# Performance work log

Hardware: AMD Instinct MI355X
Metric: run time of the kernel (lower is better)

Reference implementation:

```python
import jax, jax.numpy as jnp
import numpy as np

M = 262144      # total tokens
K = 64          # n_channels (input dim)
N = 64          # expert_size (output dim)
E = 8           # n_experts


def setup_inputs() -> dict:
    key = jax.random.key(0)
    k1, k2, k3 = jax.random.split(key, 3)
    x = jax.random.normal(k1, (M, K), dtype=jnp.float32)
    sel = jax.random.randint(k2, (M,), 0, E, dtype=jnp.int32)
    w = jax.random.normal(k3, (E, K, N), dtype=jnp.float32)
    return {"x": x, "sel": sel, "w": w}


def reference(x, sel, w):
    # cvmm: out[m] = x[m] @ w[sel[m]]  (per-token expert GEMM)
    # Loop over the small fixed expert set; accumulate masked dense GEMMs
    # instead of materializing w[sel] ([M,K,N], which would be huge).
    E_ = w.shape[0]
    out = jnp.zeros((x.shape[0], w.shape[2]), dtype=x.dtype)
    for e in range(E_):
        mask = (sel == e)[:, None]           # [M,1]
        out = out + jnp.where(mask, x @ w[e], jnp.zeros((), x.dtype))
    return out
```

## Files before the change

### kernel.cpp

```cpp
#include <hip/hip_runtime.h>


typedef __bf16 bf16x8 __attribute__((ext_vector_type(8)));
typedef float floatx4 __attribute__((ext_vector_type(4)));

#define MT_PER_BLOCK 16

__global__ __launch_bounds__(256, 4) void cvmm_kernel(
    const float* __restrict__ x,
    const int* __restrict__ sel,
    const float* __restrict__ w,
    float* __restrict__ out,
    int M)
{
    const int lane = threadIdx.x & 63;
    const int wave = threadIdx.x >> 6;
    const int n0   = wave << 4;
    const int quad = lane >> 4;
    const int l16  = lane & 15;

    bf16x8 bfrag[8][2];
#pragma unroll
    for (int e = 0; e < 8; ++e) {
#pragma unroll
        for (int t = 0; t < 2; ++t) {
            const float* wp = w + ((e * 64 + t * 32 + quad * 8) * 64) + (n0 + l16);
#pragma unroll
            for (int j = 0; j < 8; ++j) {
                bfrag[e][t][j] = (__bf16)wp[j * 64];
            }
        }
    }

    bf16x8 zf;
#pragma unroll
    for (int j = 0; j < 8; ++j) zf[j] = (__bf16)0.0f;

    const int mt0 = blockIdx.x * MT_PER_BLOCK;

    for (int i = 0; i < MT_PER_BLOCK; ++i) {
        const int m0 = (mt0 + i) << 4;
        if (m0 >= M) break;

        const int s = sel[m0 + l16];

        const float* xp = x + (size_t)(m0 + l16) * 64 + quad * 8;
        floatx4 a0lo = *(const floatx4*)(xp);
        floatx4 a0hi = *(const floatx4*)(xp + 4);
        floatx4 a1lo = *(const floatx4*)(xp + 32);
        floatx4 a1hi = *(const floatx4*)(xp + 36);

        bf16x8 af0, af1;
#pragma unroll
        for (int j = 0; j < 4; ++j) {
            af0[j]     = (__bf16)a0lo[j];
            af0[j + 4] = (__bf16)a0hi[j];
            af1[j]     = (__bf16)a1lo[j];
            af1[j + 4] = (__bf16)a1hi[j];
        }

        floatx4 c = {0.0f, 0.0f, 0.0f, 0.0f};

#pragma unroll
        for (int e = 0; e < 8; ++e) {
            const bool ok = (s == e);
            bf16x8 a0m = ok ? af0 : zf;
            bf16x8 a1m = ok ? af1 : zf;
            c = __builtin_amdgcn_mfma_f32_16x16x32_bf16(a0m, bfrag[e][0], c, 0, 0, 0);
            c = __builtin_amdgcn_mfma_f32_16x16x32_bf16(a1m, bfrag[e][1], c, 0, 0, 0);
        }

        float* op = out + (size_t)(m0 + quad * 4) * 64 + n0 + l16;
#pragma unroll
        for (int r = 0; r < 4; ++r) {
            op[(size_t)r * 64] = c[r];
        }
    }
}

extern "C" void kernel_launch(void* const* d_in, const int* in_sizes, int n_in,
                              void* d_out, int out_size, void* d_ws, size_t ws_size,
                              hipStream_t stream) {
    const float* x   = (const float*)d_in[0];
    const int*   sel = (const int*)d_in[1];
    const float* w   = (const float*)d_in[2];
    float*       out = (float*)d_out;

    const int M = in_sizes[0] / 64;
    const int mtiles = M / 16;
    const int blocks = (mtiles + MT_PER_BLOCK - 1) / MT_PER_BLOCK;

    cvmm_kernel<<<blocks, 256, 0, stream>>>(x, sel, w, out, M);
}
```

Baseline: 149.5 us.

## Prefetch next tile, split MFMA accumulators, use nontemporal stores, shrink per-block tiles

The loop now issues the loads for the next 16-row tile of x and sel before the current tile's MFMAs, so memory latency overlaps with compute. The MFMA chain is split into two independent accumulators to break the serial dependency, and outputs are written with nontemporal stores. Tiles per block drop from 16 to 4 and launch bounds move from 4 to 3, which means more blocks, each reloading the expert weights into registers. The bounds check on M was removed, so correctness relies on M being a multiple of 64.

```diff
diff --git a/kernel.cpp b/kernel.cpp
--- a/kernel.cpp
+++ b/kernel.cpp
@@ -4,9 +4,9 @@
 typedef __bf16 bf16x8 __attribute__((ext_vector_type(8)));
 typedef float floatx4 __attribute__((ext_vector_type(4)));
 
-#define MT_PER_BLOCK 16
+#define MT 4
 
-__global__ __launch_bounds__(256, 4) void cvmm_kernel(
+__global__ __launch_bounds__(256, 3) void cvmm_kernel(
     const float* __restrict__ x,
     const int* __restrict__ sel,
     const float* __restrict__ w,
@@ -36,44 +36,60 @@
 #pragma unroll
     for (int j = 0; j < 8; ++j) zf[j] = (__bf16)0.0f;
 
-    const int mt0 = blockIdx.x * MT_PER_BLOCK;
+    const int mt0 = blockIdx.x * MT;
 
-    for (int i = 0; i < MT_PER_BLOCK; ++i) {
-        const int m0 = (mt0 + i) << 4;
-        if (m0 >= M) break;
+    floatx4 pa0, pa1, pa2, pa3;
+    int ps;
+    {
+        const int m0 = mt0 << 4;
+        const float* xp = x + (size_t)(m0 + l16) * 64 + quad * 8;
+        pa0 = *(const floatx4*)(xp);
+        pa1 = *(const floatx4*)(xp + 4);
+        pa2 = *(const floatx4*)(xp + 32);
+        pa3 = *(const floatx4*)(xp + 36);
+        ps  = sel[m0 + l16];
+    }
 
-        const int s = sel[m0 + l16];
+#pragma unroll
+    for (int i = 0; i < MT; ++i) {
+        const floatx4 a0 = pa0, a1 = pa1, a2 = pa2, a3 = pa3;
+        const int s = ps;
 
-        const float* xp = x + (size_t)(m0 + l16) * 64 + quad * 8;
-        floatx4 a0lo = *(const floatx4*)(xp);
-        floatx4 a0hi = *(const floatx4*)(xp + 4);
-        floatx4 a1lo = *(const floatx4*)(xp + 32);
-        floatx4 a1hi = *(const floatx4*)(xp + 36);
+        if (i + 1 < MT) {
+            const int m0n = (mt0 + i + 1) << 4;
+            const float* xp = x + (size_t)(m0n + l16) * 64 + quad * 8;
+            pa0 = *(const floatx4*)(xp);
+            pa1 = *(const floatx4*)(xp + 4);
+            pa2 = *(const floatx4*)(xp + 32);
+            pa3 = *(const floatx4*)(xp + 36);
+            ps  = sel[m0n + l16];
+        }
 
         bf16x8 af0, af1;
 #pragma unroll
         for (int j = 0; j < 4; ++j) {
-            af0[j]     = (__bf16)a0lo[j];
-            af0[j + 4] = (__bf16)a0hi[j];
-            af1[j]     = (__bf16)a1lo[j];
-            af1[j + 4] = (__bf16)a1hi[j];
+            af0[j]     = (__bf16)a0[j];
+            af0[j + 4] = (__bf16)a1[j];
+            af1[j]     = (__bf16)a2[j];
+            af1[j + 4] = (__bf16)a3[j];
         }
 
-        floatx4 c = {0.0f, 0.0f, 0.0f, 0.0f};
-
+        floatx4 c0 = {0.0f, 0.0f, 0.0f, 0.0f};
+        floatx4 c1 = {0.0f, 0.0f, 0.0f, 0.0f};
 #pragma unroll
         for (int e = 0; e < 8; ++e) {
             const bool ok = (s == e);
             bf16x8 a0m = ok ? af0 : zf;
             bf16x8 a1m = ok ? af1 : zf;
-            c = __builtin_amdgcn_mfma_f32_16x16x32_bf16(a0m, bfrag[e][0], c, 0, 0, 0);
-            c = __builtin_amdgcn_mfma_f32_16x16x32_bf16(a1m, bfrag[e][1], c, 0, 0, 0);
+            c0 = __builtin_amdgcn_mfma_f32_16x16x32_bf16(a0m, bfrag[e][0], c0, 0, 0, 0);
+            c1 = __builtin_amdgcn_mfma_f32_16x16x32_bf16(a1m, bfrag[e][1], c1, 0, 0, 0);
         }
 
+        const int m0 = (mt0 + i) << 4;
         float* op = out + (size_t)(m0 + quad * 4) * 64 + n0 + l16;
 #pragma unroll
         for (int r = 0; r < 4; ++r) {
-            op[(size_t)r * 64] = c[r];
+            __builtin_nontemporal_store(c0[r] + c1[r], op + (size_t)r * 64);
         }
     }
 }
@@ -88,7 +104,7 @@
 
     const int M = in_sizes[0] / 64;
     const int mtiles = M / 16;
-    const int blocks = (mtiles + MT_PER_BLOCK - 1) / MT_PER_BLOCK;
+    const int blocks = (mtiles + MT - 1) / MT;
 
     cvmm_kernel<<<blocks, 256, 0, stream>>>(x, sel, w, out, M);
 }
```

New measurement: 151.0 us. Within noise of the previous version (+1.0%).
